# Performance work log

Measured on AMD Instinct MI355X. Metric: run time of the kernel, lower is better.

## Reference

```python
import jax, jax.numpy as jnp
import numpy as np

N = 100000       # nodes
E0 = 1600000     # edges without self loops
E = E0 + N       # with self loops appended (attr 0), matching add_self_loops
DIN = 128        # input_dim
HID = 64         # nb_hidden_gnn (per-head out_channels)
HEADS = 4
EMB = 128
L = 3            # nb_layer
NEG_SLOPE = 0.2
BN_EPS = 1e-5


def setup_inputs() -> dict:
    key = jax.random.key(0)
    ks = jax.random.split(key, 12)
    # edges with no self loops; self loops (i,i) appended with edge_attr 0
    row = jax.random.randint(ks[0], (E0,), 0, N)
    off = jax.random.randint(ks[1], (E0,), 1, N)
    col = (row + off) % N
    loops = jnp.arange(N, dtype=row.dtype)
    edge_index = jnp.stack([jnp.concatenate([row, loops]),
                            jnp.concatenate([col, loops])])
    edge_attr = jnp.concatenate([jax.random.normal(ks[2], (E0, 1), jnp.float32),
                                 jnp.zeros((N, 1), jnp.float32)])
    x = jax.random.normal(ks[3], (N, DIN), jnp.float32)
    HC = HEADS * HID
    linN0 = jax.random.normal(ks[4], (DIN, HC)) * HC ** -0.5
    linN_rest = jax.random.normal(ks[5], (L - 1, HID, HC)) * HC ** -0.5
    linE_all = jax.random.normal(ks[6], (L, 1, HEADS)) * HEADS ** -0.5  # nb_edge_attr=1
    att_all = jax.random.normal(ks[7], (L, HEADS, 2 * HID + 1)) * (2 * HID + 1) ** -0.5
    bias_all = jnp.zeros((L, HID))  # concat=False -> bias [out_channels]
    bn_gamma = jnp.ones((L - 1, HID))
    bn_beta = jnp.zeros((L - 1, HID))
    W = jax.random.normal(ks[8], (HID, EMB)) * HID ** -0.5
    b = jnp.zeros((EMB,))
    return {"x": x, "edge_index": edge_index, "edge_attr": edge_attr,
            "linN0": linN0, "linN_rest": linN_rest, "linE_all": linE_all,
            "att_all": att_all, "bias_all": bias_all,
            "bn_gamma": bn_gamma, "bn_beta": bn_beta, "W": W, "b": b}


def _gcn_layer(x, row, col, edge_attr, linN, linE, att, bias, bn):
    n = x.shape[0]
    if bn is not None:
        gamma, beta = bn
        mu = x.mean(axis=0)
        var = x.var(axis=0)
        x = (x - mu) * jax.lax.rsqrt(var + BN_EPS) * gamma + beta
    h = (x @ linN).reshape(n, HEADS, HID)                 # [N,H,C]
    e = (edge_attr @ linE)                                # [E,H] (nb_edge_attr=1)
    att_i = att[:, :HID]                                  # [H,C]
    att_j = att[:, HID:2 * HID]                           # [H,C]
    att_e = att[:, 2 * HID:]                              # [H,1]
    # per-node partial scores avoid gathering full features twice
    s_i = jnp.einsum('nhc,hc->nh', h, att_i)
    s_j = jnp.einsum('nhc,hc->nh', h, att_j)
    logits = s_i[row] + s_j[col] + e * att_e[:, 0]        # [E,H]
    logits = jax.nn.leaky_relu(logits, NEG_SLOPE)
    # segment softmax over destination nodes (edge_index[1])
    m = jax.ops.segment_max(logits, col, num_segments=n)
    p = jnp.exp(logits - m[col])
    denom = jax.ops.segment_sum(p, col, num_segments=n)
    alpha = p / (denom[col] + 1e-16)
    # message: alpha * x[source], scatter-add to destination
    msg = alpha[:, :, None] * h[row]                      # [E,H,C]
    out = jax.ops.segment_sum(msg, col, num_segments=n)   # [N,H,C]
    out = out.mean(axis=1) + bias + h.mean(axis=1)        # concat=False, res=True
    return jax.nn.relu(out)


def reference(x, edge_index, edge_attr, linN0, linN_rest, linE_all, att_all,
              bias_all, bn_gamma, bn_beta, W, b):
    row, col = edge_index[0], edge_index[1]
    emb = x
    for l in range(L):
        linN = linN0 if l == 0 else linN_rest[l - 1]
        bn = None if l == 0 else (bn_gamma[l - 1], bn_beta[l - 1])
        emb = _gcn_layer(emb, row, col, edge_attr, linN, linE_all[l],
                         att_all[l], bias_all[l], bn)
    return emb @ W + b
```

## Files before the change

kernel.cpp:

```cpp
#include <hip/hip_runtime.h>
#include <math.h>

#define NN 100000
#define E0E 1600000
#define EE (E0E + NN)
#define NEG 0.2f
#define BNEPS 1e-5f
#define LOG2E 1.4426950408889634f

typedef float f4 __attribute__((ext_vector_type(4)));
typedef float f2 __attribute__((ext_vector_type(2)));

__device__ __forceinline__ float wred_max(float v) {
#pragma unroll
  for (int m = 1; m < 64; m <<= 1) v = fmaxf(v, __shfl_xor(v, m, 64));
  return v;
}
__device__ __forceinline__ float wred_sum(float v) {
#pragma unroll
  for (int m = 1; m < 64; m <<= 1) v += __shfl_xor(v, m, 64);
  return v;
}
__device__ __forceinline__ float sel4(float a0, float a1, float a2, float a3, int hd) {
  return (hd & 2) ? ((hd & 1) ? a3 : a2) : ((hd & 1) ? a1 : a0);
}
__device__ __forceinline__ unsigned short f2bf(float x) {
  unsigned u = __float_as_uint(x);
  return (unsigned short)((u + 0x7fffu + ((u >> 16) & 1u)) >> 16);
}
__device__ __forceinline__ float bf2f(unsigned short s) {
  return __uint_as_float(((unsigned)s) << 16);
}

__global__ void k_zero_i32(int* p, int n) {
  int i = blockIdx.x * blockDim.x + threadIdx.x;
  if (i < n) p[i] = 0;
}
__global__ void k_zero_f64(double* p, int n) {
  int i = blockIdx.x * blockDim.x + threadIdx.x;
  if (i < n) p[i] = 0.0;
}
__global__ void k_count(const int* __restrict__ col, int* cnt, int e) {
  int i = blockIdx.x * blockDim.x + threadIdx.x;
  if (i < e) atomicAdd(&cnt[col[i]], 1);
}
#define SCAN_T 1024
__global__ void k_scan1(const int* __restrict__ cnt, int* partial, int n, int chunk) {
  int i = blockIdx.x * blockDim.x + threadIdx.x;
  int beg = i * chunk, end = min(n, beg + chunk);
  int s = 0;
  for (int j = beg; j < end; ++j) s += cnt[j];
  partial[i] = s;
}
__global__ void k_scan2(int* partial) {
  __shared__ int lds[SCAN_T];
  int t = threadIdx.x;
  int v = partial[t];
  lds[t] = v;
  __syncthreads();
  for (int off = 1; off < SCAN_T; off <<= 1) {
    int add = (t >= off) ? lds[t - off] : 0;
    __syncthreads();
    lds[t] += add;
    __syncthreads();
  }
  partial[t] = lds[t] - v;
}
__global__ void k_scan3(const int* __restrict__ cnt, const int* __restrict__ partial,
                        int* rowptr, int* cursor, int n, int chunk, int etot) {
  int i = blockIdx.x * blockDim.x + threadIdx.x;
  int beg = i * chunk, end = min(n, beg + chunk);
  int run = partial[i];
  for (int j = beg; j < end; ++j) {
    rowptr[j] = run;
    cursor[j] = run;
    run += cnt[j];
  }
  if (i == SCAN_T - 1) rowptr[n] = etot;
}
__global__ void k_scatter(const int* __restrict__ row, const int* __restrict__ col,
                          const float* __restrict__ ea, int* cursor, int2* csr, int e) {
  int i = blockIdx.x * blockDim.x + threadIdx.x;
  if (i < e) {
    int c = col[i];
    int p = atomicAdd(&cursor[c], 1);
    csr[p] = make_int2(row[i], __float_as_int(ea[i]));
  }
}

__global__ void k_bnstats(const float* __restrict__ x, double* sums, int n) {
  int f = threadIdx.x & 63;
  int rt = (blockIdx.x * blockDim.x + threadIdx.x) >> 6;
  int rstride = (gridDim.x * blockDim.x) >> 6;
  double s = 0.0, q = 0.0;
  for (int r = rt; r < n; r += rstride) {
    double v = (double)x[(size_t)r * 64 + f];
    s += v;
    q += v * v;
  }
  __shared__ double ls[256], lq[256];
  ls[threadIdx.x] = s;
  lq[threadIdx.x] = q;
  __syncthreads();
  if (threadIdx.x < 64) {
    s = ls[threadIdx.x] + ls[threadIdx.x + 64] + ls[threadIdx.x + 128] + ls[threadIdx.x + 192];
    q = lq[threadIdx.x] + lq[threadIdx.x + 64] + lq[threadIdx.x + 128] + lq[threadIdx.x + 192];
    atomicAdd(&sums[f], s);
    atomicAdd(&sums[64 + f], q);
  }
}
__global__ void k_bnfinal(const double* __restrict__ sums, const float* __restrict__ gamma,
                          const float* __restrict__ beta, float* AB, int n) {
  int f = threadIdx.x;
  if (f < 64) {
    double mean = sums[f] / n;
    double var = sums[64 + f] / n - mean * mean;
    float A = gamma[f] * rsqrtf((float)var + BNEPS);
    AB[f] = A;
    AB[64 + f] = beta[f] - (float)mean * A;
  }
}

template <int K, int COLS, bool BN, bool ATT, bool OB>
__global__ __launch_bounds__(1024) void k_lin(const float* __restrict__ x,
                                              const float* __restrict__ w,
                                              const float* __restrict__ AB,
                                              const float* __restrict__ att,
                                              const float* __restrict__ ob,
                                              void* __restrict__ houtv,
                                              float* __restrict__ s_i,
                                              float* __restrict__ s_j, int n) {
  constexpr int CPL = COLS / 64;
  constexpr int ROWS = 8;
  __shared__ float wl[K * COLS];
  for (int idx = threadIdx.x; idx < K * COLS; idx += 1024) wl[idx] = w[idx];
  __syncthreads();
  const int lane = threadIdx.x & 63;
  const int wid = threadIdx.x >> 6;
  int wgl = __builtin_amdgcn_readfirstlane(blockIdx.x * 16 + wid);
  const int wstep = gridDim.x * 16 * ROWS;
  for (int r0 = wgl * ROWS; r0 < n; r0 += wstep) {
    float acc[ROWS][CPL];
#pragma unroll
    for (int r = 0; r < ROWS; ++r)
#pragma unroll
      for (int c = 0; c < CPL; ++c) acc[r][c] = 0.f;
    const float* xr = x + (size_t)r0 * K;
#pragma unroll 4
    for (int k = 0; k < K; ++k) {
      float wv[CPL];
      if constexpr (CPL == 4) {
        f4 t = *(const f4*)&wl[k * COLS + lane * 4];
        wv[0] = t[0]; wv[1] = t[1]; wv[2] = t[2]; wv[3] = t[3];
      } else {
        f2 t = *(const f2*)&wl[k * COLS + lane * 2];
        wv[0] = t[0]; wv[1] = t[1];
      }
      float A, Bc;
      if (BN) { A = AB[k]; Bc = AB[64 + k]; }
#pragma unroll
      for (int r = 0; r < ROWS; ++r) {
        float xv = xr[r * K + k];
        if (BN) xv = fmaf(xv, A, Bc);
#pragma unroll
        for (int c = 0; c < CPL; ++c) acc[r][c] = fmaf(xv, wv[c], acc[r][c]);
      }
    }
#pragma unroll
    for (int r = 0; r < ROWS; ++r) {
      size_t rr = (size_t)(r0 + r);
      if constexpr (OB) {
        float* hout = (float*)houtv;
        f2 bv = *(const f2*)&ob[lane * 2];
        f2 o;
        o[0] = acc[r][0] + bv[0];
        o[1] = acc[r][1] + bv[1];
        *(f2*)&hout[rr * COLS + lane * 2] = o;
      } else {
        unsigned short* hout = (unsigned short*)houtv;
        f4 a;
        a[0] = acc[r][0]; a[1] = acc[r][1]; a[2] = acc[r][2]; a[3] = acc[r][3];
        ushort4 hb4;
        hb4.x = f2bf(a[0]); hb4.y = f2bf(a[1]); hb4.z = f2bf(a[2]); hb4.w = f2bf(a[3]);
        *(ushort4*)&hout[rr * COLS + lane * 4] = hb4;
        if constexpr (ATT) {
          int hd = lane >> 4, ch = (lane & 15) * 4;
          const float* ar = att + hd * 129;
          float pi = a[0] * ar[ch] + a[1] * ar[ch + 1] + a[2] * ar[ch + 2] + a[3] * ar[ch + 3];
          float pj = a[0] * ar[64 + ch] + a[1] * ar[64 + ch + 1] + a[2] * ar[64 + ch + 2] +
                     a[3] * ar[64 + ch + 3];
#pragma unroll
          for (int m = 1; m < 16; m <<= 1) {
            pi += __shfl_xor(pi, m, 64);
            pj += __shfl_xor(pj, m, 64);
          }
          if ((lane & 15) == 0) {
            s_i[rr * 4 + hd] = pi;
            s_j[rr * 4 + hd] = pj;
          }
        }
      }
    }
  }
}

__global__ __launch_bounds__(256) void k_edge(const int* __restrict__ rowptr,
                                              const int2* __restrict__ csr,
                                              const float* __restrict__ s_i,
                                              const float* __restrict__ s_j,
                                              const unsigned short* __restrict__ hb,
                                              const float* __restrict__ linE,
                                              const float* __restrict__ att,
                                              const float* __restrict__ bias,
                                              float* __restrict__ xout, int n) {
  __shared__ float lp[4][64][4];
  __shared__ int lsrc[4][64];
  const int lane = threadIdx.x & 63;
  const int wid = threadIdx.x >> 6;
  int v = blockIdx.x * 4 + wid;
  if (v >= n) return;
  v = __builtin_amdgcn_readfirstlane(v);
  const int base = rowptr[v];
  const int deg = rowptr[v + 1] - base;

  const float coef0 = linE[0] * att[0 * 129 + 128];
  const float coef1 = linE[1] * att[1 * 129 + 128];
  const float coef2 = linE[2] * att[2 * 129 + 128];
  const float coef3 = linE[3] * att[3 * 129 + 128];
  const float sj0 = s_j[(size_t)v * 4 + 0];
  const float sj1 = s_j[(size_t)v * 4 + 1];
  const float sj2 = s_j[(size_t)v * 4 + 2];
  const float sj3 = s_j[(size_t)v * 4 + 3];

  auto edge_logits = [&](int i, int& src, float& g0, float& g1, float& g2, float& g3) {
    int2 pk = csr[i];
    src = pk.x;
    float ea = __int_as_float(pk.y);
    f4 siv = *(const f4*)&s_i[(size_t)src * 4];
    g0 = siv[0] + sj0 + ea * coef0; g0 = fmaxf(g0, g0 * NEG);
    g1 = siv[1] + sj1 + ea * coef1; g1 = fmaxf(g1, g1 * NEG);
    g2 = siv[2] + sj2 + ea * coef2; g2 = fmaxf(g2, g2 * NEG);
    g3 = siv[3] + sj3 + ea * coef3; g3 = fmaxf(g3, g3 * NEG);
  };

  const int hd = lane >> 4;
  float msel, rdsel;
  bool fast = (deg <= 64);
  if (fast) {
    float g0 = -INFINITY, g1 = -INFINITY, g2 = -INFINITY, g3 = -INFINITY;
    int src = 0;
    bool valid = lane < deg;
    if (valid) edge_logits(base + lane, src, g0, g1, g2, g3);
    float m0 = wred_max(g0), m1 = wred_max(g1), m2 = wred_max(g2), m3 = wred_max(g3);
    float p0 = valid ? exp2f((g0 - m0) * LOG2E) : 0.f;
    float p1 = valid ? exp2f((g1 - m1) * LOG2E) : 0.f;
    float p2 = valid ? exp2f((g2 - m2) * LOG2E) : 0.f;
    float p3 = valid ? exp2f((g3 - m3) * LOG2E) : 0.f;
    if (valid) {
      f4 pp; pp[0] = p0; pp[1] = p1; pp[2] = p2; pp[3] = p3;
      *(f4*)&lp[wid][lane][0] = pp;
      lsrc[wid][lane] = src;
    }
    float d0 = wred_sum(p0), d1 = wred_sum(p1), d2 = wred_sum(p2), d3 = wred_sum(p3);
    rdsel = 1.f / (sel4(d0, d1, d2, d3, hd) + 1e-16f);
    msel = 0.f;
  } else {
    float m0 = -INFINITY, m1 = -INFINITY, m2 = -INFINITY, m3 = -INFINITY;
    for (int c0 = 0; c0 < deg; c0 += 64) {
      int i = c0 + lane;
      if (i < deg) {
        int src; float g0, g1, g2, g3;
        edge_logits(base + i, src, g0, g1, g2, g3);
        m0 = fmaxf(m0, g0); m1 = fmaxf(m1, g1); m2 = fmaxf(m2, g2); m3 = fmaxf(m3, g3);
      }
    }
    m0 = wred_max(m0); m1 = wred_max(m1); m2 = wred_max(m2); m3 = wred_max(m3);
    float d0 = 0, d1 = 0, d2 = 0, d3 = 0;
    for (int c0 = 0; c0 < deg; c0 += 64) {
      int i = c0 + lane;
      if (i < deg) {
        int src; float g0, g1, g2, g3;
        edge_logits(base + i, src, g0, g1, g2, g3);
        d0 += exp2f((g0 - m0) * LOG2E);
        d1 += exp2f((g1 - m1) * LOG2E);
        d2 += exp2f((g2 - m2) * LOG2E);
        d3 += exp2f((g3 - m3) * LOG2E);
      }
    }
    d0 = wred_sum(d0); d1 = wred_sum(d1); d2 = wred_sum(d2); d3 = wred_sum(d3);
    msel = sel4(m0, m1, m2, m3, hd);
    rdsel = 1.f / (sel4(d0, d1, d2, d3, hd) + 1e-16f);
  }

  f4 acc;
  {
    ushort4 hr = *(const ushort4*)&hb[(size_t)v * 256 + lane * 4];
    acc[0] = bf2f(hr.x); acc[1] = bf2f(hr.y); acc[2] = bf2f(hr.z); acc[3] = bf2f(hr.w);
  }
  if (fast) {
    for (int e = 0; e < deg; ++e) {
      int src = lsrc[wid][e];
      float a = lp[wid][e][hd] * rdsel;
      ushort4 hr = *(const ushort4*)&hb[(size_t)src * 256 + lane * 4];
      acc[0] = fmaf(a, bf2f(hr.x), acc[0]);
      acc[1] = fmaf(a, bf2f(hr.y), acc[1]);
      acc[2] = fmaf(a, bf2f(hr.z), acc[2]);
      acc[3] = fmaf(a, bf2f(hr.w), acc[3]);
    }
  } else {
    const float sjsel = sel4(sj0, sj1, sj2, sj3, hd);
    const float cfsel = sel4(coef0, coef1, coef2, coef3, hd);
    for (int e = base; e < base + deg; ++e) {
      int2 pk = csr[e];
      int src = pk.x;
      float ea = __int_as_float(pk.y);
      f4 siv = *(const f4*)&s_i[(size_t)src * 4];
      float lg = sel4(siv[0], siv[1], siv[2], siv[3], hd) + sjsel + ea * cfsel;
      lg = fmaxf(lg, lg * NEG);
      float a = exp2f((lg - msel) * LOG2E) * rdsel;
      ushort4 hr = *(const ushort4*)&hb[(size_t)src * 256 + lane * 4];
      acc[0] = fmaf(a, bf2f(hr.x), acc[0]);
      acc[1] = fmaf(a, bf2f(hr.y), acc[1]);
      acc[2] = fmaf(a, bf2f(hr.z), acc[2]);
      acc[3] = fmaf(a, bf2f(hr.w), acc[3]);
    }
  }
#pragma unroll
  for (int m = 16; m < 64; m <<= 1) {
    acc[0] += __shfl_xor(acc[0], m, 64);
    acc[1] += __shfl_xor(acc[1], m, 64);
    acc[2] += __shfl_xor(acc[2], m, 64);
    acc[3] += __shfl_xor(acc[3], m, 64);
  }
  if (lane < 16) {
    f4 bv = *(const f4*)&bias[lane * 4];
    f4 o;
#pragma unroll
    for (int c = 0; c < 4; ++c) o[c] = fmaxf(acc[c] * 0.25f + bv[c], 0.f);
    *(f4*)&xout[(size_t)v * 64 + lane * 4] = o;
  }
}

extern "C" void kernel_launch(void* const* d_in, const int* in_sizes, int n_in,
                              void* d_out, int out_size, void* d_ws, size_t ws_size,
                              hipStream_t stream) {
  const float* x_in = (const float*)d_in[0];
  const int* ei = (const int*)d_in[1];
  const float* eattr = (const float*)d_in[2];
  const float* linN0 = (const float*)d_in[3];
  const float* linNr = (const float*)d_in[4];
  const float* linE = (const float*)d_in[5];
  const float* attA = (const float*)d_in[6];
  const float* biasA = (const float*)d_in[7];
  const float* bng = (const float*)d_in[8];
  const float* bnb = (const float*)d_in[9];
  const float* W = (const float*)d_in[10];
  const float* bb = (const float*)d_in[11];
  float* out = (float*)d_out;

  const int* row = ei;
  const int* col = ei + EE;

  char* ws = (char*)d_ws;
  size_t o = 0;
  auto alloc = [&](size_t bytes) {
    void* p = ws + o;
    o += (bytes + 255) & ~(size_t)255;
    return p;
  };
  int* cnt = (int*)alloc((size_t)NN * 4);
  int* cursor = (int*)alloc((size_t)NN * 4);
  int* rowptr = (int*)alloc((size_t)(NN + 1) * 4);
  int* partial = (int*)alloc((size_t)SCAN_T * 4);
  int2* csr = (int2*)alloc((size_t)EE * 8);
  unsigned short* h = (unsigned short*)alloc((size_t)NN * 256 * 2);
  float* si = (float*)alloc((size_t)NN * 4 * 4);
  float* sj = (float*)alloc((size_t)NN * 4 * 4);
  float* xa = (float*)alloc((size_t)NN * 64 * 4);
  float* xb = (float*)alloc((size_t)NN * 64 * 4);
  double* bnsum = (double*)alloc(256 * 8);
  float* AB = (float*)alloc(128 * 4);
  if (o > ws_size) return;

  const int chunk = (NN + SCAN_T - 1) / SCAN_T;
  const int LIN_GRID = ((NN / 8) + 15) / 16;

  k_zero_i32<<<(NN + 255) / 256, 256, 0, stream>>>(cnt, NN);
  k_zero_f64<<<1, 256, 0, stream>>>(bnsum, 256);
  k_count<<<(EE + 255) / 256, 256, 0, stream>>>(col, cnt, EE);
  k_scan1<<<4, 256, 0, stream>>>(cnt, partial, NN, chunk);
  k_scan2<<<1, SCAN_T, 0, stream>>>(partial);
  k_scan3<<<4, 256, 0, stream>>>(cnt, partial, rowptr, cursor, NN, chunk, EE);
  k_scatter<<<(EE + 255) / 256, 256, 0, stream>>>(row, col, eattr, cursor, csr, EE);

  k_lin<128, 256, false, true, false><<<LIN_GRID, 1024, 0, stream>>>(
      x_in, linN0, nullptr, attA + 0, nullptr, h, si, sj, NN);
  k_edge<<<NN / 4, 256, 0, stream>>>(rowptr, csr, si, sj, h, linE + 0, attA + 0, biasA + 0, xa, NN);

  k_bnstats<<<256, 256, 0, stream>>>(xa, bnsum, NN);
  k_bnfinal<<<1, 64, 0, stream>>>(bnsum, bng + 0, bnb + 0, AB, NN);
  k_lin<64, 256, true, true, false><<<LIN_GRID, 1024, 0, stream>>>(
      xa, linNr + 0, AB, attA + 516, nullptr, h, si, sj, NN);
  k_edge<<<NN / 4, 256, 0, stream>>>(rowptr, csr, si, sj, h, linE + 4, attA + 516, biasA + 64, xb, NN);

  k_bnstats<<<256, 256, 0, stream>>>(xb, bnsum + 128, NN);
  k_bnfinal<<<1, 64, 0, stream>>>(bnsum + 128, bng + 64, bnb + 64, AB, NN);
  k_lin<64, 256, true, true, false><<<LIN_GRID, 1024, 0, stream>>>(
      xb, linNr + 64 * 256, AB, attA + 2 * 516, nullptr, h, si, sj, NN);
  k_edge<<<NN / 4, 256, 0, stream>>>(rowptr, csr, si, sj, h, linE + 8, attA + 2 * 516, biasA + 128, xa, NN);

  k_lin<64, 128, false, false, true><<<LIN_GRID, 1024, 0, stream>>>(
      xa, W, nullptr, nullptr, bb, out, nullptr, nullptr, NN);
}
```

Baseline: 1.012 ms.

## Replace scalar FMA linear layers with bf16 MFMA GEMM and folded batch-norm weights

Replaces the fp32 FMA-based node linear kernel with a bf16 MFMA 16x16x32 GEMM. A small prep kernel transposes the weights and converts them to bf16, folding the batch-norm scale into the weights and the shift into a per-column bias vector. Input rows are converted to bf16 and staged in XOR-swizzled LDS tiles, and the attention dot products are fused into the epilogue. This targets the dense projection cost at the price of bf16 rounding of the inputs and weights, plus one extra tiny launch per layer.

After: 940.1 us. -7.1%, faster.

```diff
diff --git a/kernel.cpp b/kernel.cpp
--- a/kernel.cpp
+++ b/kernel.cpp
@@ -10,6 +10,7 @@
 
 typedef float f4 __attribute__((ext_vector_type(4)));
 typedef float f2 __attribute__((ext_vector_type(2)));
+typedef short s8v __attribute__((ext_vector_type(8)));
 
 __device__ __forceinline__ float wred_max(float v) {
 #pragma unroll
@@ -121,83 +122,145 @@
   }
 }
 
-template <int K, int COLS, bool BN, bool ATT, bool OB>
-__global__ __launch_bounds__(1024) void k_lin(const float* __restrict__ x,
-                                              const float* __restrict__ w,
-                                              const float* __restrict__ AB,
-                                              const float* __restrict__ att,
-                                              const float* __restrict__ ob,
-                                              void* __restrict__ houtv,
-                                              float* __restrict__ s_i,
-                                              float* __restrict__ s_j, int n) {
-  constexpr int CPL = COLS / 64;
-  constexpr int ROWS = 8;
-  __shared__ float wl[K * COLS];
-  for (int idx = threadIdx.x; idx < K * COLS; idx += 1024) wl[idx] = w[idx];
-  __syncthreads();
+__global__ void k_prepw(const float* __restrict__ W, const float* __restrict__ AB,
+                        const float* __restrict__ bin, unsigned short* __restrict__ Wt,
+                        float* __restrict__ cvec, int K, int N, int mode) {
+  int n = threadIdx.x;
+  if (n >= N) return;
+  float c = (mode == 2) ? bin[n] : 0.f;
+  for (int k = 0; k < K; ++k) {
+    float w = W[k * N + n];
+    float a = 1.f, b = 0.f;
+    if (mode == 1) { a = AB[k]; b = AB[64 + k]; }
+    Wt[n * K + k] = f2bf(a * w);
+    c = fmaf(b, w, c);
+  }
+  cvec[n] = c;
+}
+
+template <int K, int CT, bool ATT, bool OB>
+__global__ __launch_bounds__(256, 2) void k_gemm(const float* __restrict__ x,
+                                                 const unsigned short* __restrict__ Wt,
+                                                 const float* __restrict__ cvec,
+                                                 const float* __restrict__ att,
+                                                 void* __restrict__ houtv,
+                                                 float* __restrict__ s_i,
+                                                 float* __restrict__ s_j, int n,
+                                                 int ntiles) {
+  constexpr int KS = K / 32;
+  constexpr int ROWB = 2 * K;
+  constexpr int CPR = K / 8;
+  constexpr int NCOL = 4 * CT * 16;
+  __shared__ unsigned char xs[64 * ROWB];
   const int lane = threadIdx.x & 63;
-  const int wid = threadIdx.x >> 6;
-  int wgl = __builtin_amdgcn_readfirstlane(blockIdx.x * 16 + wid);
-  const int wstep = gridDim.x * 16 * ROWS;
-  for (int r0 = wgl * ROWS; r0 < n; r0 += wstep) {
-    float acc[ROWS][CPL];
-#pragma unroll
-    for (int r = 0; r < ROWS; ++r)
-#pragma unroll
-      for (int c = 0; c < CPL; ++c) acc[r][c] = 0.f;
-    const float* xr = x + (size_t)r0 * K;
-#pragma unroll 4
-    for (int k = 0; k < K; ++k) {
-      float wv[CPL];
-      if constexpr (CPL == 4) {
-        f4 t = *(const f4*)&wl[k * COLS + lane * 4];
-        wv[0] = t[0]; wv[1] = t[1]; wv[2] = t[2]; wv[3] = t[3];
-      } else {
-        f2 t = *(const f2*)&wl[k * COLS + lane * 2];
-        wv[0] = t[0]; wv[1] = t[1];
-      }
-      float A, Bc;
-      if (BN) { A = AB[k]; Bc = AB[64 + k]; }
-#pragma unroll
-      for (int r = 0; r < ROWS; ++r) {
-        float xv = xr[r * K + k];
-        if (BN) xv = fmaf(xv, A, Bc);
-#pragma unroll
-        for (int c = 0; c < CPL; ++c) acc[r][c] = fmaf(xv, wv[c], acc[r][c]);
-      }
-    }
-#pragma unroll
-    for (int r = 0; r < ROWS; ++r) {
-      size_t rr = (size_t)(r0 + r);
+  const int wv = threadIdx.x >> 6;
+  const int l15 = lane & 15;
+  const int lq = lane >> 4;
+  const int colbase = wv * CT * 16;
+
+  s8v wfr[CT][KS];
+#pragma unroll
+  for (int ct = 0; ct < CT; ++ct)
+#pragma unroll
+    for (int ks = 0; ks < KS; ++ks)
+      wfr[ct][ks] = *(const s8v*)&Wt[(size_t)(colbase + ct * 16 + l15) * K + ks * 32 + lq * 8];
+  float cb[CT][4];
+#pragma unroll
+  for (int ct = 0; ct < CT; ++ct)
+#pragma unroll
+    for (int r = 0; r < 4; ++r) cb[ct][r] = cvec[colbase + ct * 16 + lq * 4 + r];
+  float ati[ATT ? CT : 1][4], atj[ATT ? CT : 1][4];
+  if constexpr (ATT) {
+    const float* ar = att + wv * 129;
+#pragma unroll
+    for (int ct = 0; ct < CT; ++ct)
+#pragma unroll
+      for (int r = 0; r < 4; ++r) {
+        int cc = ct * 16 + lq * 4 + r;
+        ati[ct][r] = ar[cc];
+        atj[ct][r] = ar[64 + cc];
+      }
+  }
+
+  for (int t = blockIdx.x; t < ntiles; t += gridDim.x) {
+    const int row0 = t * 64;
+    __syncthreads();
+#pragma unroll
+    for (int i = 0; i < (64 * CPR) / 256; ++i) {
+      int c = threadIdx.x + i * 256;
+      int row = c / CPR, kc = c % CPR;
+      int rg = min(row0 + row, n - 1);
+      const float* xp = x + (size_t)rg * K + kc * 8;
+      f4 a0 = *(const f4*)xp;
+      f4 a1 = *(const f4*)(xp + 4);
+      union { s8v v; unsigned short u[8]; } pk;
+      pk.u[0] = f2bf(a0[0]); pk.u[1] = f2bf(a0[1]); pk.u[2] = f2bf(a0[2]); pk.u[3] = f2bf(a0[3]);
+      pk.u[4] = f2bf(a1[0]); pk.u[5] = f2bf(a1[1]); pk.u[6] = f2bf(a1[2]); pk.u[7] = f2bf(a1[3]);
+      *(s8v*)&xs[row * ROWB + ((kc * 16) ^ ((row & 7) << 4))] = pk.v;
+    }
+    __syncthreads();
+    f4 acc[4][CT];
+#pragma unroll
+    for (int rt = 0; rt < 4; ++rt)
+#pragma unroll
+      for (int ct = 0; ct < CT; ++ct) acc[rt][ct] = (f4)0.f;
+#pragma unroll
+    for (int ks = 0; ks < KS; ++ks) {
+      s8v xf[4];
+#pragma unroll
+      for (int rt = 0; rt < 4; ++rt) {
+        int row = rt * 16 + l15;
+        int kb = ks * 64 + lq * 16;
+        xf[rt] = *(const s8v*)&xs[row * ROWB + (kb ^ ((row & 7) << 4))];
+      }
+#pragma unroll
+      for (int rt = 0; rt < 4; ++rt)
+#pragma unroll
+        for (int ct = 0; ct < CT; ++ct)
+          acc[rt][ct] = __builtin_amdgcn_mfma_f32_16x16x32_bf16(wfr[ct][ks], xf[rt],
+                                                                acc[rt][ct], 0, 0, 0);
+    }
+#pragma unroll
+    for (int rt = 0; rt < 4; ++rt) {
+      if (row0 + rt * 16 >= n) continue;
+      const size_t xrow = (size_t)(row0 + rt * 16 + l15);
+      float v[CT][4];
+#pragma unroll
+      for (int ct = 0; ct < CT; ++ct)
+#pragma unroll
+        for (int r = 0; r < 4; ++r) v[ct][r] = acc[rt][ct][r] + cb[ct][r];
       if constexpr (OB) {
-        float* hout = (float*)houtv;
-        f2 bv = *(const f2*)&ob[lane * 2];
-        f2 o;
-        o[0] = acc[r][0] + bv[0];
-        o[1] = acc[r][1] + bv[1];
-        *(f2*)&hout[rr * COLS + lane * 2] = o;
+        float* outp = (float*)houtv;
+#pragma unroll
+        for (int ct = 0; ct < CT; ++ct) {
+          f4 o;
+          o[0] = v[ct][0]; o[1] = v[ct][1]; o[2] = v[ct][2]; o[3] = v[ct][3];
+          *(f4*)&outp[xrow * NCOL + colbase + ct * 16 + lq * 4] = o;
+        }
       } else {
         unsigned short* hout = (unsigned short*)houtv;
-        f4 a;
-        a[0] = acc[r][0]; a[1] = acc[r][1]; a[2] = acc[r][2]; a[3] = acc[r][3];
-        ushort4 hb4;
-        hb4.x = f2bf(a[0]); hb4.y = f2bf(a[1]); hb4.z = f2bf(a[2]); hb4.w = f2bf(a[3]);
-        *(ushort4*)&hout[rr * COLS + lane * 4] = hb4;
-        if constexpr (ATT) {
-          int hd = lane >> 4, ch = (lane & 15) * 4;
-          const float* ar = att + hd * 129;
-          float pi = a[0] * ar[ch] + a[1] * ar[ch + 1] + a[2] * ar[ch + 2] + a[3] * ar[ch + 3];
-          float pj = a[0] * ar[64 + ch] + a[1] * ar[64 + ch + 1] + a[2] * ar[64 + ch + 2] +
-                     a[3] * ar[64 + ch + 3];
-#pragma unroll
-          for (int m = 1; m < 16; m <<= 1) {
-            pi += __shfl_xor(pi, m, 64);
-            pj += __shfl_xor(pj, m, 64);
+#pragma unroll
+        for (int ct = 0; ct < CT; ++ct) {
+          ushort4 hb4;
+          hb4.x = f2bf(v[ct][0]); hb4.y = f2bf(v[ct][1]);
+          hb4.z = f2bf(v[ct][2]); hb4.w = f2bf(v[ct][3]);
+          *(ushort4*)&hout[xrow * NCOL + colbase + ct * 16 + lq * 4] = hb4;
+        }
+      }
+      if constexpr (ATT) {
+        float pi = 0.f, pj = 0.f;
+#pragma unroll
+        for (int ct = 0; ct < CT; ++ct)
+#pragma unroll
+          for (int r = 0; r < 4; ++r) {
+            pi = fmaf(v[ct][r], ati[ct][r], pi);
+            pj = fmaf(v[ct][r], atj[ct][r], pj);
           }
-          if ((lane & 15) == 0) {
-            s_i[rr * 4 + hd] = pi;
-            s_j[rr * 4 + hd] = pj;
-          }
+        pi += __shfl_xor(pi, 16, 64); pi += __shfl_xor(pi, 32, 64);
+        pj += __shfl_xor(pj, 16, 64); pj += __shfl_xor(pj, 32, 64);
+        if (lane < 16) {
+          s_i[xrow * 4 + wv] = pi;
+          s_j[xrow * 4 + wv] = pj;
         }
       }
     }
@@ -380,10 +443,13 @@
   float* xb = (float*)alloc((size_t)NN * 64 * 4);
   double* bnsum = (double*)alloc(256 * 8);
   float* AB = (float*)alloc(128 * 4);
+  unsigned short* Wt = (unsigned short*)alloc((size_t)256 * 128 * 2);
+  float* cvec = (float*)alloc(256 * 4);
   if (o > ws_size) return;
 
   const int chunk = (NN + SCAN_T - 1) / SCAN_T;
-  const int LIN_GRID = ((NN / 8) + 15) / 16;
+  const int NTILES = (NN + 63) / 64;
+  const int GG = 521;
 
   k_zero_i32<<<(NN + 255) / 256, 256, 0, stream>>>(cnt, NN);
   k_zero_f64<<<1, 256, 0, stream>>>(bnsum, 256);
@@ -393,22 +459,26 @@
   k_scan3<<<4, 256, 0, stream>>>(cnt, partial, rowptr, cursor, NN, chunk, EE);
   k_scatter<<<(EE + 255) / 256, 256, 0, stream>>>(row, col, eattr, cursor, csr, EE);
 
-  k_lin<128, 256, false, true, false><<<LIN_GRID, 1024, 0, stream>>>(
-      x_in, linN0, nullptr, attA + 0, nullptr, h, si, sj, NN);
+  k_prepw<<<1, 256, 0, stream>>>(linN0, nullptr, nullptr, Wt, cvec, 128, 256, 0);
+  k_gemm<128, 4, true, false><<<GG, 256, 0, stream>>>(x_in, Wt, cvec, attA + 0, h, si, sj,
+                                                      NN, NTILES);
   k_edge<<<NN / 4, 256, 0, stream>>>(rowptr, csr, si, sj, h, linE + 0, attA + 0, biasA + 0, xa, NN);
 
   k_bnstats<<<256, 256, 0, stream>>>(xa, bnsum, NN);
   k_bnfinal<<<1, 64, 0, stream>>>(bnsum, bng + 0, bnb + 0, AB, NN);
-  k_lin<64, 256, true, true, false><<<LIN_GRID, 1024, 0, stream>>>(
-      xa, linNr + 0, AB, attA + 516, nullptr, h, si, sj, NN);
+  k_prepw<<<1, 256, 0, stream>>>(linNr, AB, nullptr, Wt, cvec, 64, 256, 1);
+  k_gemm<64, 4, true, false><<<GG, 256, 0, stream>>>(xa, Wt, cvec, attA + 516, h, si, sj,
+                                                     NN, NTILES);
   k_edge<<<NN / 4, 256, 0, stream>>>(rowptr, csr, si, sj, h, linE + 4, attA + 516, biasA + 64, xb, NN);
 
   k_bnstats<<<256, 256, 0, stream>>>(xb, bnsum + 128, NN);
   k_bnfinal<<<1, 64, 0, stream>>>(bnsum + 128, bng + 64, bnb + 64, AB, NN);
-  k_lin<64, 256, true, true, false><<<LIN_GRID, 1024, 0, stream>>>(
-      xb, linNr + 64 * 256, AB, attA + 2 * 516, nullptr, h, si, sj, NN);
+  k_prepw<<<1, 256, 0, stream>>>(linNr + 64 * 256, AB, nullptr, Wt, cvec, 64, 256, 1);
+  k_gemm<64, 4, true, false><<<GG, 256, 0, stream>>>(xb, Wt, cvec, attA + 2 * 516, h, si, sj,
+                                                     NN, NTILES);
   k_edge<<<NN / 4, 256, 0, stream>>>(rowptr, csr, si, sj, h, linE + 8, attA + 2 * 516, biasA + 128, xa, NN);
 
-  k_lin<64, 128, false, false, true><<<LIN_GRID, 1024, 0, stream>>>(
-      xa, W, nullptr, nullptr, bb, out, nullptr, nullptr, NN);
-}
+  k_prepw<<<1, 256, 0, stream>>>(W, nullptr, bb, Wt, cvec, 64, 128, 2);
+  k_gemm<64, 2, false, true><<<GG, 256, 0, stream>>>(xa, Wt, cvec, nullptr, out, nullptr,
+                                                     nullptr, NN, NTILES);
+}
```
